# Kernel optimization log

Measured on AMD Instinct MI355X. Metric: run time of the kernel, lower is better.

Reference implementation:

```python
import jax, jax.numpy as jnp
import numpy as np

F = 50          # num features
CARD = 10000    # cardinality per feature
D = 64          # factor_dim
A = 64          # attention_size
IU, JU = np.triu_indices(F, k=1)  # upper-triangular pair indices, P = F*(F-1)/2


def setup_inputs() -> dict:
    key = jax.random.key(0)
    ks = jax.random.split(key, 8)
    inputs = jax.random.randint(ks[0], (1024, F), 0, CARD, dtype=jnp.int32)
    emb_table = jax.random.normal(ks[1], (F * CARD, D), dtype=jnp.float32) * 0.05
    w_lin = jax.random.normal(ks[2], (F * CARD,), dtype=jnp.float32) * 0.05
    b_lin = jnp.zeros((1,), dtype=jnp.float32)
    W1 = jax.random.normal(ks[3], (D, A), dtype=jnp.float32) * (1.0 / np.sqrt(D))
    b1 = jnp.zeros((A,), dtype=jnp.float32)
    W2 = jax.random.normal(ks[4], (A, 1), dtype=jnp.float32) * (1.0 / np.sqrt(A))
    b2 = jnp.zeros((1,), dtype=jnp.float32)
    return {"inputs": inputs, "emb_table": emb_table, "w_lin": w_lin,
            "b_lin": b_lin, "W1": W1, "b1": b1, "W2": W2, "b2": b2}


def reference(inputs, emb_table, w_lin, b_lin, W1, b1, W2, b2):
    # Per-feature tables are stacked into one flat table; offset indices per feature.
    flat_idx = inputs + (jnp.arange(F, dtype=jnp.int32) * CARD)[None, :]  # [B, F]
    line_out = jnp.sum(w_lin[flat_idx], axis=1, keepdims=True) + b_lin    # [B, 1]
    factor = emb_table[flat_idx]                                          # [B, F, D]
    # Upper-triangular pairwise element-wise products (i < j), P = F(F-1)/2
    inter = factor[:, IU, :] * factor[:, JU, :]                           # [B, P, D]
    # Attention: Dense(A) -> ReLU -> Dense(1) -> Softmax over pairs
    h = jax.nn.relu(jnp.einsum('bpd,da->bpa', inter, W1) + b1)            # [B, P, A]
    logits = jnp.einsum('bpa,ao->bpo', h, W2) + b2                        # [B, P, 1]
    scores = jax.nn.softmax(logits, axis=1)                               # [B, P, 1]
    pooled = jnp.sum(inter, axis=-1, keepdims=True)                       # [B, P, 1]
    return line_out + jnp.sum(pooled * scores, axis=1)                    # [B, 1]
```

## Files before the change

### kernel.cpp

```cpp
#include <hip/hip_runtime.h>
#include <math.h>

#define FN 50
#define CARD 10000
#define NP 1225
#define NTILE 77
#define NPAD (NTILE*16)
#define FSTRIDE 72

typedef _Float16 half8 __attribute__((ext_vector_type(8)));
typedef __fp16 half2t __attribute__((ext_vector_type(2)));
typedef __fp16 half4t __attribute__((ext_vector_type(4)));
typedef float floatx4 __attribute__((ext_vector_type(4)));

static __device__ __forceinline__ half2t h2max0(half2t v) {
  half2t r;
  r[0] = v[0] > (__fp16)0 ? v[0] : (__fp16)0;
  r[1] = v[1] > (__fp16)0 ? v[1] : (__fp16)0;
  return r;
}
static __device__ __forceinline__ float hdot2(half2t a, half2t b, float c) {
#if __has_builtin(__builtin_amdgcn_fdot2)
  return __builtin_amdgcn_fdot2(a, b, c, false);
#else
  return c + (float)a[0]*(float)b[0] + (float)a[1]*(float)b[1];
#endif
}

__global__ __launch_bounds__(256, 4)
void afm_kernel(const int* __restrict__ inp,
                const float* __restrict__ emb,
                const float* __restrict__ wlin,
                const float* __restrict__ blin,
                const float* __restrict__ W1,
                const float* __restrict__ b1,
                const float* __restrict__ W2,
                const float* __restrict__ b2,
                float* __restrict__ out)
{
  __shared__ __align__(16) _Float16 s_fac[FN][FSTRIDE];
  __shared__ __align__(16) _Float16 s_w1[512 * 8];
  __shared__ __align__(16) unsigned s_pij[NPAD];
  __shared__ __align__(16) __fp16 s_lg4[NPAD * 4];
  __shared__ float s_pool[NPAD];
  __shared__ float s_wl[FN];
  __shared__ float s_red[8];

  const int tid  = threadIdx.x;
  const int b    = blockIdx.x;
  const int lane = tid & 63;
  const int wave = tid >> 6;
  const int c    = lane & 15;
  const int kq   = lane >> 4;

  for (int p = tid; p < NPAD; p += 256) {
    int pp = p < NP ? p : NP - 1;
    int i = (int)((99.0f - sqrtf(9801.0f - 8.0f * (float)pp)) * 0.5f);
    if (i < 0) i = 0;
    while ((i + 1) * (98 - i) / 2 <= pp) ++i;
    while (i > 0 && i * (99 - i) / 2 > pp) --i;
    int j = pp - i * (99 - i) / 2 + i + 1;
    s_pij[p] = (unsigned)(i * (FSTRIDE * 2)) | ((unsigned)(j * (FSTRIDE * 2)) << 16);
  }

  const int* inprow = inp + b * FN;
  for (int idx = tid; idx < FN * 16; idx += 256) {
    int f = idx >> 4, q = idx & 15;
    int flat = inprow[f] + f * CARD;
    floatx4 v = ((const floatx4*)emb)[(long)flat * 16 + q];
    half2t lo = __builtin_amdgcn_cvt_pkrtz(v[0], v[1]);
    half2t hi = __builtin_amdgcn_cvt_pkrtz(v[2], v[3]);
    half4t pk = {lo[0], lo[1], hi[0], hi[1]};
    *(half4t*)&s_fac[f][q * 4] = pk;
  }
  if (tid < FN) {
    int flat = inprow[tid] + tid * CARD;
    s_wl[tid] = wlin[flat];
  }

  for (int ch = tid; ch < 512; ch += 256) {
    int ks = ch >> 8, mt = (ch >> 6) & 3, ln = ch & 63;
    int cc = ln & 15, kk = ln >> 4;
    __fp16 tmp[8];
#pragma unroll
    for (int j = 0; j < 4; ++j) {
      float x = W1[(ks * 32 + kk * 8 + 2 * j)     * 64 + mt * 16 + cc];
      float y = W1[(ks * 32 + kk * 8 + 2 * j + 1) * 64 + mt * 16 + cc];
      half2t hw = __builtin_amdgcn_cvt_pkrtz(x, y);
      tmp[2 * j] = hw[0]; tmp[2 * j + 1] = hw[1];
    }
    *(half8*)&s_w1[ch * 8] = *(const half8*)tmp;
  }

  floatx4 bias[4];
  half2t w2h[4][2];
#pragma unroll
  for (int mt = 0; mt < 4; ++mt) {
    bias[mt] = ((const floatx4*)b1)[mt * 4 + kq];
    floatx4 wv = ((const floatx4*)W2)[mt * 4 + kq];
    w2h[mt][0] = __builtin_amdgcn_cvt_pkrtz(wv[0], wv[1]);
    w2h[mt][1] = __builtin_amdgcn_cvt_pkrtz(wv[2], wv[3]);
  }
  _Float16 onev = (c == 0) ? (_Float16)1 : (_Float16)0;
  half8 onesf = {onev, onev, onev, onev, onev, onev, onev, onev};

  __syncthreads();

#define LDW1(ks, mt) (*(const half8*)&s_w1[(((ks) * 4 + (mt)) * 64 + lane) * 8])
  const char* fbase = (const char*)&s_fac[0][0];
  const int koff = kq * 16;
  {
    int t = wave;
    int pcur = t * 16 + c;
    unsigned po = s_pij[pcur];
    int offi = (int)(po & 0xffffu) + koff;
    int offj = (int)(po >> 16) + koff;
    half8 cvi0 = *(const half8*)(fbase + offi);
    half8 cvj0 = *(const half8*)(fbase + offj);
    half8 cvi1 = *(const half8*)(fbase + offi + 64);
    half8 cvj1 = *(const half8*)(fbase + offj + 64);

    while (true) {
      int tn = t + 4;
      int pn = tn * 16 + c; if (pn > NPAD - 1) pn = NPAD - 1;
      unsigned pon = s_pij[pn];

      half8 pr0 = cvi0 * cvj0;
      half8 pr1 = cvi1 * cvj1;

      floatx4 acc[4];
#pragma unroll
      for (int mt = 0; mt < 4; ++mt) {
        acc[mt] = __builtin_amdgcn_mfma_f32_16x16x32_f16(LDW1(0, mt), pr0, bias[mt], 0, 0, 0);
        acc[mt] = __builtin_amdgcn_mfma_f32_16x16x32_f16(LDW1(1, mt), pr1, acc[mt], 0, 0, 0);
      }
      floatx4 accp = __builtin_amdgcn_mfma_f32_16x16x32_f16(onesf, pr0, (floatx4){0.f,0.f,0.f,0.f}, 0, 0, 0);
      accp = __builtin_amdgcn_mfma_f32_16x16x32_f16(onesf, pr1, accp, 0, 0, 0);

      int offi_n = (int)(pon & 0xffffu) + koff;
      int offj_n = (int)(pon >> 16) + koff;
      cvi0 = *(const half8*)(fbase + offi_n);
      cvj0 = *(const half8*)(fbase + offj_n);
      cvi1 = *(const half8*)(fbase + offi_n + 64);
      cvj1 = *(const half8*)(fbase + offj_n + 64);

      float lg = 0.f;
#pragma unroll
      for (int mt = 0; mt < 4; ++mt) {
        half2t h0 = __builtin_amdgcn_cvt_pkrtz(acc[mt][0], acc[mt][1]);
        half2t h1 = __builtin_amdgcn_cvt_pkrtz(acc[mt][2], acc[mt][3]);
        h0 = h2max0(h0);
        h1 = h2max0(h1);
        lg = hdot2(h0, w2h[mt][0], lg);
        lg = hdot2(h1, w2h[mt][1], lg);
      }
      s_lg4[pcur * 4 + kq] = (__fp16)lg;
      if (kq == 0) s_pool[pcur] = accp[0];

      t = tn;
      if (t >= NTILE) break;
      pcur = t * 16 + c;
    }
  }
#undef LDW1

  __syncthreads();

  float se = 0.f, spe = 0.f;
  for (int p = tid; p < NP; p += 256) {
    half4t v = *(const half4t*)&s_lg4[p * 4];
    float lg = ((float)v[0] + (float)v[1]) + ((float)v[2] + (float)v[3]);
    float e = __expf(lg);
    se += e;
    spe += e * s_pool[p];
  }
#pragma unroll
  for (int o = 32; o; o >>= 1) {
    se  += __shfl_xor(se, o, 64);
    spe += __shfl_xor(spe, o, 64);
  }
  if (lane == 0) { s_red[wave] = se; s_red[4 + wave] = spe; }
  __syncthreads();
  if (tid == 0) {
    float line = blin[0];
#pragma unroll
    for (int f = 0; f < FN; ++f) line += s_wl[f];
    float SE  = s_red[0] + s_red[1] + s_red[2] + s_red[3];
    float SPE = s_red[4] + s_red[5] + s_red[6] + s_red[7];
    out[b] = line + SPE / SE;
  }
}

extern "C" void kernel_launch(void* const* d_in, const int* in_sizes, int n_in,
                              void* d_out, int out_size, void* d_ws, size_t ws_size,
                              hipStream_t stream) {
  const int*   inp  = (const int*)d_in[0];
  const float* emb  = (const float*)d_in[1];
  const float* wlin = (const float*)d_in[2];
  const float* blin = (const float*)d_in[3];
  const float* W1   = (const float*)d_in[4];
  const float* b1   = (const float*)d_in[5];
  const float* W2   = (const float*)d_in[6];
  const float* b2   = (const float*)d_in[7];
  float* outp = (float*)d_out;
  const int B = in_sizes[0] / FN;
  afm_kernel<<<B, 256, 0, stream>>>(inp, emb, wlin, blin, W1, b1, W2, b2, outp);
}
```

Baseline: 24.08 us.

## Fuse softmax accumulation into MFMA loop and prefetch pair indices two tiles ahead

Reduces the four per-quadrant logit partials with cross-lane shuffles inside the main loop, then applies exp and accumulates the softmax sums in registers. This removes the shared-memory logit and pool buffers, one block-wide barrier and the separate reduction pass. The pair-index lookup is also loaded two tiles ahead to hide LDS latency. In exchange the loop gains shuffles and an exp per iteration, and the final reduction now mixes only the 16 column lanes. The logits also stay in fp32 instead of being rounded to fp16.

```diff
diff --git a/kernel.cpp b/kernel.cpp
--- a/kernel.cpp
+++ b/kernel.cpp
@@ -41,8 +41,6 @@
   __shared__ __align__(16) _Float16 s_fac[FN][FSTRIDE];
   __shared__ __align__(16) _Float16 s_w1[512 * 8];
   __shared__ __align__(16) unsigned s_pij[NPAD];
-  __shared__ __align__(16) __fp16 s_lg4[NPAD * 4];
-  __shared__ float s_pool[NPAD];
   __shared__ float s_wl[FN];
   __shared__ float s_red[8];
 
@@ -109,21 +107,23 @@
 #define LDW1(ks, mt) (*(const half8*)&s_w1[(((ks) * 4 + (mt)) * 64 + lane) * 8])
   const char* fbase = (const char*)&s_fac[0][0];
   const int koff = kq * 16;
+  float se = 0.f, spe = 0.f;
   {
     int t = wave;
     int pcur = t * 16 + c;
-    unsigned po = s_pij[pcur];
-    int offi = (int)(po & 0xffffu) + koff;
-    int offj = (int)(po >> 16) + koff;
+    unsigned po_cur = s_pij[pcur];
+    int pn1 = (t + 4) * 16 + c; if (pn1 > NPAD - 1) pn1 = NPAD - 1;
+    unsigned po_nx = s_pij[pn1];
+    int offi = (int)(po_cur & 0xffffu) + koff;
+    int offj = (int)(po_cur >> 16) + koff;
     half8 cvi0 = *(const half8*)(fbase + offi);
     half8 cvj0 = *(const half8*)(fbase + offj);
     half8 cvi1 = *(const half8*)(fbase + offi + 64);
     half8 cvj1 = *(const half8*)(fbase + offj + 64);
 
     while (true) {
-      int tn = t + 4;
-      int pn = tn * 16 + c; if (pn > NPAD - 1) pn = NPAD - 1;
-      unsigned pon = s_pij[pn];
+      int pn2 = (t + 8) * 16 + c; if (pn2 > NPAD - 1) pn2 = NPAD - 1;
+      unsigned po_n2 = s_pij[pn2];
 
       half8 pr0 = cvi0 * cvj0;
       half8 pr1 = cvi1 * cvj1;
@@ -137,8 +137,8 @@
       floatx4 accp = __builtin_amdgcn_mfma_f32_16x16x32_f16(onesf, pr0, (floatx4){0.f,0.f,0.f,0.f}, 0, 0, 0);
       accp = __builtin_amdgcn_mfma_f32_16x16x32_f16(onesf, pr1, accp, 0, 0, 0);
 
-      int offi_n = (int)(pon & 0xffffu) + koff;
-      int offj_n = (int)(pon >> 16) + koff;
+      int offi_n = (int)(po_nx & 0xffffu) + koff;
+      int offj_n = (int)(po_nx >> 16) + koff;
       cvi0 = *(const half8*)(fbase + offi_n);
       cvj0 = *(const half8*)(fbase + offj_n);
       cvi1 = *(const half8*)(fbase + offi_n + 64);
@@ -154,28 +154,24 @@
         lg = hdot2(h0, w2h[mt][0], lg);
         lg = hdot2(h1, w2h[mt][1], lg);
       }
-      s_lg4[pcur * 4 + kq] = (__fp16)lg;
-      if (kq == 0) s_pool[pcur] = accp[0];
-
-      t = tn;
+      lg += __shfl_xor(lg, 16, 64);
+      lg += __shfl_xor(lg, 32, 64);
+      float e = __expf(lg);
+      if (kq == 0 && pcur < NP) {
+        se  += e;
+        spe += e * accp[0];
+      }
+
+      t += 4;
       if (t >= NTILE) break;
       pcur = t * 16 + c;
+      po_nx = po_n2;
     }
   }
 #undef LDW1
 
-  __syncthreads();
-
-  float se = 0.f, spe = 0.f;
-  for (int p = tid; p < NP; p += 256) {
-    half4t v = *(const half4t*)&s_lg4[p * 4];
-    float lg = ((float)v[0] + (float)v[1]) + ((float)v[2] + (float)v[3]);
-    float e = __expf(lg);
-    se += e;
-    spe += e * s_pool[p];
-  }
-#pragma unroll
-  for (int o = 32; o; o >>= 1) {
+#pragma unroll
+  for (int o = 1; o <= 8; o <<= 1) {
     se  += __shfl_xor(se, o, 64);
     spe += __shfl_xor(spe, o, 64);
   }
```

After: 24.02 us (median of 2 runs). Within noise of the previous version (-0.3%).
